# Optimization experiments

Measured on AMD Instinct MI355X. Metric: run time of the kernel, lower is better.

Reference implementation:

```python
import jax, jax.numpy as jnp
import numpy as np

LOG2 = 0.6931471824645996  # float32 log(2), shifted-softplus offset

def ssp(v):
    return jax.nn.softplus(v) - LOG2

def setup_inputs() -> dict:
    key = jax.random.key(0)
    ks = jax.random.split(key, 8)
    B, A, N = 4, 512, 128
    n_in = n_factors = n_out = 256
    s_in = 1.0 / np.sqrt(n_in)
    s_f = 1.0 / np.sqrt(n_factors)
    return {
        "x": jax.random.normal(ks[0], (B, A, n_in), dtype=jnp.float32),
        "r_ij": jax.random.uniform(ks[1], (B, A, N), dtype=jnp.float32) * 5.0,
        "pairwise_mask": jnp.ones((B, A, N), dtype=jnp.float32),
        "in2f_w": jax.random.normal(ks[2], (n_in, n_factors), dtype=jnp.float32) * s_in,
        "in2f_b": jnp.zeros((n_factors,), dtype=jnp.float32),
        "f2out_w": jax.random.normal(ks[3], (n_factors, n_out), dtype=jnp.float32) * s_f,
        "f2out_b": jnp.zeros((n_out,), dtype=jnp.float32),
        "fw1": jax.random.normal(ks[4], (1, n_factors), dtype=jnp.float32),
        "fb1": jnp.zeros((n_factors,), dtype=jnp.float32),
        "fw2": jax.random.normal(ks[5], (n_factors, n_factors), dtype=jnp.float32) * s_f,
        "fb2": jnp.zeros((n_factors,), dtype=jnp.float32),
        "neighbors": jax.random.randint(ks[6], (B, A, N), 0, A, dtype=jnp.int64),
    }

def reference(x, r_ij, pairwise_mask, in2f_w, in2f_b, f2out_w, f2out_b,
              fw1, fb1, fw2, fb2, neighbors):
    # f_ij = r_ij.unsqueeze(-1); filter network: Dense+ssp -> Dense
    f_ij = r_ij[..., None]                                  # [B,A,N,1]
    W = ssp(f_ij @ fw1 + fb1) @ fw2 + fb2                   # [B,A,N,F]
    facts = x @ in2f_w + in2f_b                             # [B,A,F]
    B, A, N = neighbors.shape
    F = facts.shape[-1]
    # gather neighbor features along atom axis
    idx = neighbors.reshape(B, A * N)[..., None]            # [B,A*N,1]
    xj = jnp.take_along_axis(facts, idx, axis=1).reshape(B, A, N, F)
    xi = facts[:, :, None, :]                               # [B,A,1,F]
    y = xi * W * xj                                         # [B,A,N,F]
    y = ssp(y @ f2out_w + f2out_b)                          # [B,A,N,n_out]
    return y
```

## Files before the change

kernel.cpp:

```cpp
#include <hip/hip_runtime.h>
#include <hip/hip_bf16.h>
#include <stdint.h>

typedef unsigned short u16;

#define Adim 512
#define Ndim 128
#define Fdim 256
#define BA 2048

#define HS 264
#define XS 264

#define GRID 512
#define ITEMS 8

typedef __attribute__((ext_vector_type(8))) __bf16 bf16x8;
typedef __attribute__((ext_vector_type(4))) float f32x4;

__device__ __forceinline__ float bf2f(u16 u){
  uint32_t v = ((uint32_t)u) << 16;
  return __builtin_bit_cast(float, v);
}
__device__ __forceinline__ uint32_t cvtpk(float lo, float hi){
  uint32_t r;
  asm("v_cvt_pk_bf16_f32 %0, %1, %2" : "=v"(r) : "v"(lo), "v"(hi));
  return r;
}
__device__ __forceinline__ u16 f2bf(float f){ return (u16)cvtpk(f, f); }
__device__ __forceinline__ float ssp_f(float v){
  float m = fmaxf(v, 0.f);
  float e = __expf(-fabsf(v));
  return m + __logf(1.f + e) - 0.69314718f;
}

__global__ __launch_bounds__(256) void prep_kernel(
    const float* __restrict__ s0, u16* __restrict__ d0,
    const float* __restrict__ s1, u16* __restrict__ d1,
    const float* __restrict__ s2, u16* __restrict__ d2)
{
  __shared__ float tile[32][33];
  const float* src = (blockIdx.y == 0) ? s0 : (blockIdx.y == 1 ? s1 : s2);
  u16* dst = (blockIdx.y == 0) ? d0 : (blockIdx.y == 1 ? d1 : d2);
  int bx = (blockIdx.x & 7) * 32, by = (int)(blockIdx.x >> 3) * 32;
  int tx = threadIdx.x & 31, ty = threadIdx.x >> 5;
  #pragma unroll
  for (int r = 0; r < 4; r++)
    tile[ty + r*8][tx] = src[(size_t)(by + ty + r*8)*Fdim + bx + tx];
  __syncthreads();
  #pragma unroll
  for (int r = 0; r < 4; r++)
    dst[(size_t)(bx + ty + r*8)*Fdim + by + tx] = f2bf(tile[tx][ty + r*8]);
}

__global__ __launch_bounds__(256, 2) void facts_kernel(
    const float* __restrict__ x, const u16* __restrict__ wT,
    const float* __restrict__ bias, u16* __restrict__ facts)
{
  __shared__ __align__(16) u16 Xs[64*HS];
  const int tid = threadIdx.x;
  const int row0 = blockIdx.x * 64;

  #pragma unroll
  for (int i = 0; i < 16; i++){
    int id = i*256 + tid;
    int r = id >> 6, c4 = id & 63;
    float4 v = *(const float4*)(x + (size_t)(row0 + r)*Fdim + c4*4);
    uint2 q;
    q.x = cvtpk(v.x, v.y);
    q.y = cvtpk(v.z, v.w);
    *(uint2*)(Xs + r*HS + c4*4) = q;
  }
  __syncthreads();

  const int lane = tid & 63, wid = tid >> 6;
  const int wcol = wid * 64;
  const int l16 = lane & 15, quad = lane >> 4;

  f32x4 acc[4][4];
  #pragma unroll
  for (int mt = 0; mt < 4; mt++)
    #pragma unroll
    for (int ct = 0; ct < 4; ct++)
      acc[mt][ct] = (f32x4){0.f,0.f,0.f,0.f};

  const u16* wbase = wT + (size_t)(wcol + l16)*Fdim + quad*8;
  bf16x8 bb[2][4];
  #pragma unroll
  for (int ct = 0; ct < 4; ct++) bb[0][ct] = *(const bf16x8*)(wbase + ct*16*Fdim);

  for (int kk = 0; kk < 8; kk++){
    if (kk < 7){
      #pragma unroll
      for (int ct = 0; ct < 4; ct++)
        bb[(kk+1)&1][ct] = *(const bf16x8*)(wbase + ct*16*Fdim + (kk+1)*32);
    }
    bf16x8 af[4];
    #pragma unroll
    for (int mt = 0; mt < 4; mt++)
      af[mt] = *(const bf16x8*)(Xs + (mt*16 + l16)*HS + kk*32 + quad*8);
    #pragma unroll
    for (int mt = 0; mt < 4; mt++)
      #pragma unroll
      for (int ct = 0; ct < 4; ct++)
        acc[mt][ct] = __builtin_amdgcn_mfma_f32_16x16x32_bf16(af[mt], bb[kk&1][ct], acc[mt][ct], 0, 0, 0);
  }

  #pragma unroll
  for (int ct = 0; ct < 4; ct++){
    int f = wcol + ct*16 + l16;
    float bv = bias[f];
    #pragma unroll
    for (int mt = 0; mt < 4; mt++)
      #pragma unroll
      for (int i = 0; i < 4; i++){
        int m = mt*16 + quad*4 + i;
        facts[(size_t)(row0 + m)*Fdim + f] = f2bf(acc[mt][ct][i] + bv);
      }
  }
}

__global__ __launch_bounds__(512, 2) void fused_kernel(
    const float* __restrict__ r_ij, const u16* __restrict__ facts,
    const u16* __restrict__ fw2T, const u16* __restrict__ f2outT,
    const float* __restrict__ fw1, const float* __restrict__ fb1,
    const float* __restrict__ fb2, const float* __restrict__ f2out_b,
    const int* __restrict__ neighbors, float* __restrict__ out)
{
  __shared__ __align__(16) u16 Hs[64*HS];
  __shared__ __align__(16) u16 XJ[64*XS];
  __shared__ __align__(16) u16 Ys[64*HS];
  __shared__ int   nb_s[64];
  __shared__ float r_s[64];

  const int tid  = threadIdx.x;
  const int lane = tid & 63, wid = tid >> 6;
  const int l16  = lane & 15, quad = lane >> 4;
  const int wcol = wid * 32;
  const int g    = tid & 31;
  const int rsub = tid >> 5;

  float fw1v[8], fb1v[8];
  *(float4*)(fw1v)   = *(const float4*)(fw1 + g*8);
  *(float4*)(fw1v+4) = *(const float4*)(fw1 + g*8 + 4);
  *(float4*)(fb1v)   = *(const float4*)(fb1 + g*8);
  *(float4*)(fb1v+4) = *(const float4*)(fb1 + g*8 + 4);
  float fb2v[2], obv[2];
  #pragma unroll
  for (int ct = 0; ct < 2; ct++){
    int f = wcol + ct*16 + l16;
    fb2v[ct] = fb2[f];
    obv[ct]  = f2out_b[f];
  }

  const u16* w1base = fw2T   + (size_t)(wcol + l16)*Fdim + quad*8;
  const u16* w2base = f2outT + (size_t)(wcol + l16)*Fdim + quad*8;

  f32x4 acc[4][2];
  #pragma unroll
  for (int mt = 0; mt < 4; mt++)
    #pragma unroll
    for (int ct = 0; ct < 2; ct++)
      acc[mt][ct] = (f32x4){0.f,0.f,0.f,0.f};

  bf16x8 bw[4][2];

  {
    const int item0 = blockIdx.x;
    const int pair0 = item0 >> 1, half0 = item0 & 1;
    if (tid < 64){
      nb_s[tid] = neighbors[(size_t)pair0*Ndim + half0*64 + tid];
      r_s[tid]  = r_ij[(size_t)pair0*Ndim + half0*64 + tid];
    }
  }
  __syncthreads();

  for (int l = 0; l < ITEMS; l++){
    const int item = l*GRID + blockIdx.x;
    const int pair = item >> 1;
    const int half = item & 1;
    const int bbase = (pair >> 9) << 9;

    #pragma unroll
    for (int kk = 0; kk < 4; kk++)
      #pragma unroll
      for (int ct = 0; ct < 2; ct++)
        bw[kk][ct] = *(const bf16x8*)(w1base + ct*16*Fdim + kk*32);

    float4 gx[4];
    #pragma unroll
    for (int i = 0; i < 4; i++){
      int row = i*16 + rsub;
      gx[i] = *(const float4*)(facts + ((size_t)(bbase + nb_s[row]))*Fdim + g*8);
    }

    int nb_nxt = 0; float r_nxt = 0.f;
    if (l + 1 < ITEMS && tid < 64){
      const int item1 = (l+1)*GRID + blockIdx.x;
      const int pair1 = item1 >> 1, half1 = item1 & 1;
      nb_nxt = neighbors[(size_t)pair1*Ndim + half1*64 + tid];
      r_nxt  = r_ij[(size_t)pair1*Ndim + half1*64 + tid];
    }

    float xif[2];
    #pragma unroll
    for (int ct = 0; ct < 2; ct++)
      xif[ct] = bf2f(facts[(size_t)pair*Fdim + wcol + ct*16 + l16]);

    #pragma unroll
    for (int i = 0; i < 4; i++){
      int row = i*16 + rsub;
      float rv = r_s[row];
      float h[8];
      #pragma unroll
      for (int j = 0; j < 8; j++)
        h[j] = ssp_f(fmaf(rv, fw1v[j], fb1v[j]));
      uint4 pw;
      pw.x = cvtpk(h[0], h[1]);
      pw.y = cvtpk(h[2], h[3]);
      pw.z = cvtpk(h[4], h[5]);
      pw.w = cvtpk(h[6], h[7]);
      *(uint4*)(Hs + row*HS + g*8) = pw;
    }

    #pragma unroll
    for (int i = 0; i < 4; i++){
      int row = i*16 + rsub;
      *(float4*)(XJ + row*XS + g*8) = gx[i];
    }
    __syncthreads();

    if (l + 1 < ITEMS && tid < 64){
      nb_s[tid] = nb_nxt;
      r_s[tid]  = r_nxt;
    }

    #pragma unroll
    for (int kk = 0; kk < 4; kk++){
      bf16x8 af[4];
      #pragma unroll
      for (int mt = 0; mt < 4; mt++)
        af[mt] = *(const bf16x8*)(Hs + (mt*16 + l16)*HS + kk*32 + quad*8);
      #pragma unroll
      for (int mt = 0; mt < 4; mt++)
        #pragma unroll
        for (int ct = 0; ct < 2; ct++)
          acc[mt][ct] = __builtin_amdgcn_mfma_f32_16x16x32_bf16(af[mt], bw[kk][ct], acc[mt][ct], 0, 0, 0);
    }
    __builtin_amdgcn_sched_barrier(0);
    #pragma unroll
    for (int kk = 0; kk < 4; kk++)
      #pragma unroll
      for (int ct = 0; ct < 2; ct++)
        bw[kk][ct] = *(const bf16x8*)(w1base + ct*16*Fdim + (kk+4)*32);
    #pragma unroll
    for (int kk = 0; kk < 4; kk++){
      bf16x8 af[4];
      #pragma unroll
      for (int mt = 0; mt < 4; mt++)
        af[mt] = *(const bf16x8*)(Hs + (mt*16 + l16)*HS + (kk+4)*32 + quad*8);
      #pragma unroll
      for (int mt = 0; mt < 4; mt++)
        #pragma unroll
        for (int ct = 0; ct < 2; ct++)
          acc[mt][ct] = __builtin_amdgcn_mfma_f32_16x16x32_bf16(af[mt], bw[kk][ct], acc[mt][ct], 0, 0, 0);
    }

    #pragma unroll
    for (int kk = 0; kk < 4; kk++)
      #pragma unroll
      for (int ct = 0; ct < 2; ct++)
        bw[kk][ct] = *(const bf16x8*)(w2base + ct*16*Fdim + kk*32);

    #pragma unroll
    for (int ct = 0; ct < 2; ct++){
      int f = wcol + ct*16 + l16;
      #pragma unroll
      for (int mt = 0; mt < 4; mt++){
        #pragma unroll
        for (int i = 0; i < 4; i++){
          int m = mt*16 + quad*4 + i;
          float wv = acc[mt][ct][i] + fb2v[ct];
          float y  = xif[ct] * wv * bf2f(XJ[m*XS + f]);
          Ys[m*HS + f] = f2bf(y);
          acc[mt][ct][i] = 0.f;
        }
      }
    }
    __syncthreads();

    #pragma unroll
    for (int kk = 0; kk < 4; kk++){
      bf16x8 af[4];
      #pragma unroll
      for (int mt = 0; mt < 4; mt++)
        af[mt] = *(const bf16x8*)(Ys + (mt*16 + l16)*HS + kk*32 + quad*8);
      #pragma unroll
      for (int mt = 0; mt < 4; mt++)
        #pragma unroll
        for (int ct = 0; ct < 2; ct++)
          acc[mt][ct] = __builtin_amdgcn_mfma_f32_16x16x32_bf16(af[mt], bw[kk][ct], acc[mt][ct], 0, 0, 0);
    }
    __builtin_amdgcn_sched_barrier(0);
    #pragma unroll
    for (int kk = 0; kk < 4; kk++)
      #pragma unroll
      for (int ct = 0; ct < 2; ct++)
        bw[kk][ct] = *(const bf16x8*)(w2base + ct*16*Fdim + (kk+4)*32);
    #pragma unroll
    for (int kk = 0; kk < 4; kk++){
      bf16x8 af[4];
      #pragma unroll
      for (int mt = 0; mt < 4; mt++)
        af[mt] = *(const bf16x8*)(Ys + (mt*16 + l16)*HS + (kk+4)*32 + quad*8);
      #pragma unroll
      for (int mt = 0; mt < 4; mt++)
        #pragma unroll
        for (int ct = 0; ct < 2; ct++)
          acc[mt][ct] = __builtin_amdgcn_mfma_f32_16x16x32_bf16(af[mt], bw[kk][ct], acc[mt][ct], 0, 0, 0);
    }

    size_t obase = ((size_t)pair * Ndim + half*64) * Fdim;
    #pragma unroll
    for (int ct = 0; ct < 2; ct++){
      int f = wcol + ct*16 + l16;
      #pragma unroll
      for (int mt = 0; mt < 4; mt++){
        #pragma unroll
        for (int i = 0; i < 4; i++){
          int m = mt*16 + quad*4 + i;
          __builtin_nontemporal_store(ssp_f(acc[mt][ct][i] + obv[ct]),
                                      out + obase + (size_t)m*Fdim + f);
          acc[mt][ct][i] = 0.f;
        }
      }
    }
  }
}

extern "C" void kernel_launch(void* const* d_in, const int* in_sizes, int n_in,
                              void* d_out, int out_size, void* d_ws, size_t ws_size,
                              hipStream_t stream)
{
  const float* x        = (const float*)d_in[0];
  const float* r_ij     = (const float*)d_in[1];
  const float* in2f_w   = (const float*)d_in[3];
  const float* in2f_b   = (const float*)d_in[4];
  const float* f2out_w  = (const float*)d_in[5];
  const float* f2out_b  = (const float*)d_in[6];
  const float* fw1      = (const float*)d_in[7];
  const float* fb1      = (const float*)d_in[8];
  const float* fw2      = (const float*)d_in[9];
  const float* fb2      = (const float*)d_in[10];
  const int*   neighbors= (const int*)d_in[11];
  float* out = (float*)d_out;

  u16* facts  = (u16*)d_ws;
  u16* in2fT  = (u16*)((char*)d_ws + (1u<<20));
  u16* fw2T   = (u16*)((char*)d_ws + (1u<<20) + 1*(1u<<17));
  u16* f2outT = (u16*)((char*)d_ws + (1u<<20) + 2*(1u<<17));

  prep_kernel<<<dim3(64, 3), 256, 0, stream>>>(in2f_w, in2fT, fw2, fw2T, f2out_w, f2outT);
  facts_kernel<<<32, 256, 0, stream>>>(x, in2fT, in2f_b, facts);
  fused_kernel<<<GRID, 512, 0, stream>>>(r_ij, facts, fw2T, f2outT,
                                         fw1, fb1, fb2, f2out_b, neighbors, out);
}
```

Measured before the change: 433.8 us.

## Software-pipeline fused kernel: prefetch next neighbor gather and defer output epilogue

Restructures the per-item loop into a software pipeline. XJ and the neighbor/r buffers are double-buffered so the next item's neighbor gather is issued one iteration ahead, and the H filter tile for the next item is computed in the current iteration. The second GEMM's accumulator is kept separate (accZ), so the softplus-and-store epilogue of the previous item runs at the start of the next iteration and overlaps with MFMA work. This is meant to hide global gather latency and store cost, at the price of more LDS (a second XJ buffer) and more registers, which could reduce occupancy under the 2-blocks-per-SM launch bound.

Measured after the change: 491.5 us. 1.13x slower.

```diff
diff --git a/kernel.cpp b/kernel.cpp
--- a/kernel.cpp
+++ b/kernel.cpp
@@ -128,10 +128,10 @@
     const int* __restrict__ neighbors, float* __restrict__ out)
 {
   __shared__ __align__(16) u16 Hs[64*HS];
-  __shared__ __align__(16) u16 XJ[64*XS];
+  __shared__ __align__(16) u16 XJ[2][64*XS];
   __shared__ __align__(16) u16 Ys[64*HS];
-  __shared__ int   nb_s[64];
-  __shared__ float r_s[64];
+  __shared__ int   nb_s[2][64];
+  __shared__ float r_s[2][64];
 
   const int tid  = threadIdx.x;
   const int lane = tid & 63, wid = tid >> 6;
@@ -156,61 +156,40 @@
   const u16* w1base = fw2T   + (size_t)(wcol + l16)*Fdim + quad*8;
   const u16* w2base = f2outT + (size_t)(wcol + l16)*Fdim + quad*8;
 
-  f32x4 acc[4][2];
+  f32x4 accW[4][2], accZ[4][2];
   #pragma unroll
   for (int mt = 0; mt < 4; mt++)
     #pragma unroll
-    for (int ct = 0; ct < 2; ct++)
-      acc[mt][ct] = (f32x4){0.f,0.f,0.f,0.f};
+    for (int ct = 0; ct < 2; ct++){
+      accW[mt][ct] = (f32x4){0.f,0.f,0.f,0.f};
+      accZ[mt][ct] = (f32x4){0.f,0.f,0.f,0.f};
+    }
 
   bf16x8 bw[4][2];
 
   {
-    const int item0 = blockIdx.x;
-    const int pair0 = item0 >> 1, half0 = item0 & 1;
+    const int it0 = blockIdx.x;
+    const int p0 = it0 >> 1, h0 = it0 & 1;
     if (tid < 64){
-      nb_s[tid] = neighbors[(size_t)pair0*Ndim + half0*64 + tid];
-      r_s[tid]  = r_ij[(size_t)pair0*Ndim + half0*64 + tid];
+      nb_s[0][tid] = neighbors[(size_t)p0*Ndim + h0*64 + tid];
+      r_s[0][tid]  = r_ij[(size_t)p0*Ndim + h0*64 + tid];
     }
   }
   __syncthreads();
-
-  for (int l = 0; l < ITEMS; l++){
-    const int item = l*GRID + blockIdx.x;
-    const int pair = item >> 1;
-    const int half = item & 1;
-    const int bbase = (pair >> 9) << 9;
-
-    #pragma unroll
-    for (int kk = 0; kk < 4; kk++)
-      #pragma unroll
-      for (int ct = 0; ct < 2; ct++)
-        bw[kk][ct] = *(const bf16x8*)(w1base + ct*16*Fdim + kk*32);
-
-    float4 gx[4];
+  {
+    const int it0 = blockIdx.x;
+    const int p0 = it0 >> 1;
+    const int bb0 = (p0 >> 9) << 9;
+    float4 g0[4];
     #pragma unroll
     for (int i = 0; i < 4; i++){
       int row = i*16 + rsub;
-      gx[i] = *(const float4*)(facts + ((size_t)(bbase + nb_s[row]))*Fdim + g*8);
-    }
-
-    int nb_nxt = 0; float r_nxt = 0.f;
-    if (l + 1 < ITEMS && tid < 64){
-      const int item1 = (l+1)*GRID + blockIdx.x;
-      const int pair1 = item1 >> 1, half1 = item1 & 1;
-      nb_nxt = neighbors[(size_t)pair1*Ndim + half1*64 + tid];
-      r_nxt  = r_ij[(size_t)pair1*Ndim + half1*64 + tid];
-    }
-
-    float xif[2];
-    #pragma unroll
-    for (int ct = 0; ct < 2; ct++)
-      xif[ct] = bf2f(facts[(size_t)pair*Fdim + wcol + ct*16 + l16]);
-
+      g0[i] = *(const float4*)(facts + ((size_t)(bb0 + nb_s[0][row]))*Fdim + g*8);
+    }
     #pragma unroll
     for (int i = 0; i < 4; i++){
       int row = i*16 + rsub;
-      float rv = r_s[row];
+      float rv = r_s[0][row];
       float h[8];
       #pragma unroll
       for (int j = 0; j < 8; j++)
@@ -222,17 +201,75 @@
       pw.w = cvtpk(h[6], h[7]);
       *(uint4*)(Hs + row*HS + g*8) = pw;
     }
-
     #pragma unroll
     for (int i = 0; i < 4; i++){
       int row = i*16 + rsub;
-      *(float4*)(XJ + row*XS + g*8) = gx[i];
-    }
-    __syncthreads();
-
-    if (l + 1 < ITEMS && tid < 64){
-      nb_s[tid] = nb_nxt;
-      r_s[tid]  = r_nxt;
+      *(float4*)(XJ[0] + row*XS + g*8) = g0[i];
+    }
+    if (tid < 64){
+      const int it1 = GRID + blockIdx.x;
+      const int p1 = it1 >> 1, h1 = it1 & 1;
+      nb_s[1][tid] = neighbors[(size_t)p1*Ndim + h1*64 + tid];
+      r_s[1][tid]  = r_ij[(size_t)p1*Ndim + h1*64 + tid];
+    }
+  }
+  __syncthreads();
+
+  for (int l = 0; l < ITEMS; l++){
+    const int item = l*GRID + blockIdx.x;
+    const int pair = item >> 1;
+    const int half = item & 1;
+    const int pa = l & 1, pb = (l+1) & 1;
+
+    #pragma unroll
+    for (int kk = 0; kk < 4; kk++)
+      #pragma unroll
+      for (int ct = 0; ct < 2; ct++)
+        bw[kk][ct] = *(const bf16x8*)(w1base + ct*16*Fdim + kk*32);
+
+    float4 gx[4];
+    if (l + 1 < ITEMS){
+      const int it1 = (l+1)*GRID + blockIdx.x;
+      const int p1 = it1 >> 1;
+      const int bb1 = (p1 >> 9) << 9;
+      #pragma unroll
+      for (int i = 0; i < 4; i++){
+        int row = i*16 + rsub;
+        gx[i] = *(const float4*)(facts + ((size_t)(bb1 + nb_s[pb][row]))*Fdim + g*8);
+      }
+    }
+
+    int nb_nxt = 0; float r_nxt = 0.f;
+    if (l + 2 < ITEMS && tid < 64){
+      const int it2 = (l+2)*GRID + blockIdx.x;
+      const int p2i = it2 >> 1, h2 = it2 & 1;
+      nb_nxt = neighbors[(size_t)p2i*Ndim + h2*64 + tid];
+      r_nxt  = r_ij[(size_t)p2i*Ndim + h2*64 + tid];
+    }
+
+    float xif[2];
+    #pragma unroll
+    for (int ct = 0; ct < 2; ct++)
+      xif[ct] = bf2f(facts[(size_t)pair*Fdim + wcol + ct*16 + l16]);
+
+    if (l > 0){
+      const int pit = item - GRID;
+      const int pp = pit >> 1, ph = pit & 1;
+      size_t ob = ((size_t)pp * Ndim + ph*64) * Fdim;
+      #pragma unroll
+      for (int ct = 0; ct < 2; ct++){
+        int f = wcol + ct*16 + l16;
+        #pragma unroll
+        for (int mt = 0; mt < 4; mt++){
+          #pragma unroll
+          for (int i = 0; i < 4; i++){
+            int m = mt*16 + quad*4 + i;
+            __builtin_nontemporal_store(ssp_f(accZ[mt][ct][i] + obv[ct]),
+                                        out + ob + (size_t)m*Fdim + f);
+            accZ[mt][ct][i] = 0.f;
+          }
+        }
+      }
     }
 
     #pragma unroll
@@ -245,7 +282,14 @@
       for (int mt = 0; mt < 4; mt++)
         #pragma unroll
         for (int ct = 0; ct < 2; ct++)
-          acc[mt][ct] = __builtin_amdgcn_mfma_f32_16x16x32_bf16(af[mt], bw[kk][ct], acc[mt][ct], 0, 0, 0);
+          accW[mt][ct] = __builtin_amdgcn_mfma_f32_16x16x32_bf16(af[mt], bw[kk][ct], accW[mt][ct], 0, 0, 0);
+    }
+    if (l + 1 < ITEMS){
+      #pragma unroll
+      for (int i = 0; i < 4; i++){
+        int row = i*16 + rsub;
+        *(float4*)(XJ[pb] + row*XS + g*8) = gx[i];
+      }
     }
     __builtin_amdgcn_sched_barrier(0);
     #pragma unroll
@@ -263,9 +307,14 @@
       for (int mt = 0; mt < 4; mt++)
         #pragma unroll
         for (int ct = 0; ct < 2; ct++)
-          acc[mt][ct] = __builtin_amdgcn_mfma_f32_16x16x32_bf16(af[mt], bw[kk][ct], acc[mt][ct], 0, 0, 0);
-    }
-
+          accW[mt][ct] = __builtin_amdgcn_mfma_f32_16x16x32_bf16(af[mt], bw[kk][ct], accW[mt][ct], 0, 0, 0);
+    }
+    __syncthreads();
+
+    if (l + 2 < ITEMS && tid < 64){
+      nb_s[pa][tid] = nb_nxt;
+      r_s[pa][tid]  = r_nxt;
+    }
     #pragma unroll
     for (int kk = 0; kk < 4; kk++)
       #pragma unroll
@@ -280,11 +329,29 @@
         #pragma unroll
         for (int i = 0; i < 4; i++){
           int m = mt*16 + quad*4 + i;
-          float wv = acc[mt][ct][i] + fb2v[ct];
-          float y  = xif[ct] * wv * bf2f(XJ[m*XS + f]);
+          float wv = accW[mt][ct][i] + fb2v[ct];
+          float y  = xif[ct] * wv * bf2f(XJ[pa][m*XS + f]);
           Ys[m*HS + f] = f2bf(y);
-          acc[mt][ct][i] = 0.f;
+          accW[mt][ct][i] = 0.f;
         }
+      }
+    }
+
+    if (l + 1 < ITEMS){
+      #pragma unroll
+      for (int i = 0; i < 4; i++){
+        int row = i*16 + rsub;
+        float rv = r_s[pb][row];
+        float h[8];
+        #pragma unroll
+        for (int j = 0; j < 8; j++)
+          h[j] = ssp_f(fmaf(rv, fw1v[j], fb1v[j]));
+        uint4 pw;
+        pw.x = cvtpk(h[0], h[1]);
+        pw.y = cvtpk(h[2], h[3]);
+        pw.z = cvtpk(h[4], h[5]);
+        pw.w = cvtpk(h[6], h[7]);
+        *(uint4*)(Hs + row*HS + g*8) = pw;
       }
     }
     __syncthreads();
@@ -299,7 +366,7 @@
       for (int mt = 0; mt < 4; mt++)
         #pragma unroll
         for (int ct = 0; ct < 2; ct++)
-          acc[mt][ct] = __builtin_amdgcn_mfma_f32_16x16x32_bf16(af[mt], bw[kk][ct], acc[mt][ct], 0, 0, 0);
+          accZ[mt][ct] = __builtin_amdgcn_mfma_f32_16x16x32_bf16(af[mt], bw[kk][ct], accZ[mt][ct], 0, 0, 0);
     }
     __builtin_amdgcn_sched_barrier(0);
     #pragma unroll
@@ -317,10 +384,14 @@
       for (int mt = 0; mt < 4; mt++)
         #pragma unroll
         for (int ct = 0; ct < 2; ct++)
-          acc[mt][ct] = __builtin_amdgcn_mfma_f32_16x16x32_bf16(af[mt], bw[kk][ct], acc[mt][ct], 0, 0, 0);
-    }
-
-    size_t obase = ((size_t)pair * Ndim + half*64) * Fdim;
+          accZ[mt][ct] = __builtin_amdgcn_mfma_f32_16x16x32_bf16(af[mt], bw[kk][ct], accZ[mt][ct], 0, 0, 0);
+    }
+  }
+
+  {
+    const int item = (ITEMS-1)*GRID + blockIdx.x;
+    const int pp = item >> 1, ph = item & 1;
+    size_t ob = ((size_t)pp * Ndim + ph*64) * Fdim;
     #pragma unroll
     for (int ct = 0; ct < 2; ct++){
       int f = wcol + ct*16 + l16;
@@ -329,9 +400,8 @@
         #pragma unroll
         for (int i = 0; i < 4; i++){
           int m = mt*16 + quad*4 + i;
-          __builtin_nontemporal_store(ssp_f(acc[mt][ct][i] + obv[ct]),
-                                      out + obase + (size_t)m*Fdim + f);
-          acc[mt][ct][i] = 0.f;
+          __builtin_nontemporal_store(ssp_f(accZ[mt][ct][i] + obv[ct]),
+                                      out + ob + (size_t)m*Fdim + f);
         }
       }
     }
```
